# Kernel tuning notes

Hardware: AMD Instinct MI355X
Metric: run time of the kernel (lower is better)

## Reference

```python
import jax, jax.numpy as jnp
import numpy as np

ENC, DEC, B, S = 1024, 1024, 32, 2048


def setup_inputs() -> dict:
    key = jax.random.key(0)
    k1, k2, k3, k4, k5, k6 = jax.random.split(key, 6)
    scale_attn = 1.0 / np.sqrt(ENC + DEC)
    return {
        "decoder_hidden": jax.random.normal(k1, (B, DEC), dtype=jnp.float32),
        "encoder_outputs": jax.random.normal(k2, (B, S, ENC), dtype=jnp.float32),
        "mask": jax.random.randint(k3, (B, S), 0, 2, dtype=jnp.int32),
        "W_attn": jax.random.normal(k4, (ENC + DEC, DEC), dtype=jnp.float32) * scale_attn,
        "b_attn": jax.random.normal(k5, (DEC,), dtype=jnp.float32) * 0.02,
        "v_w": jax.random.normal(k6, (DEC,), dtype=jnp.float32) * (1.0 / np.sqrt(DEC)),
    }


def reference(decoder_hidden, encoder_outputs, mask, W_attn, b_attn, v_w):
    # Split cat((dec_exp, enc)) @ W into two GEMMs (same math, no repeat/concat).
    dec_dim = decoder_hidden.shape[-1]
    W_dec = W_attn[:dec_dim]      # [DEC, DEC]
    W_enc = W_attn[dec_dim:]      # [ENC, DEC]
    dec_proj = decoder_hidden @ W_dec                      # [B, DEC]
    enc_proj = jnp.einsum("bse,ed->bsd", encoder_outputs, W_enc)  # [B, S, DEC]
    energy = jnp.tanh(dec_proj[:, None, :] + enc_proj + b_attn)   # [B, S, DEC]
    scores = jnp.einsum("bsd,d->bs", energy, v_w)                 # [B, S]
    scores = jnp.where(mask == 0, -1e9, scores)
    attn_weights = jax.nn.softmax(scores, axis=1)                 # [B, S]
    context = jnp.einsum("bs,bse->be", attn_weights, encoder_outputs)  # [B, ENC]
    return (context, attn_weights)
```

## Files before the change

kernel.cpp:

```cpp
#include <hip/hip_runtime.h>
#include <hip/hip_bf16.h>
#include <cstdint>


#define ENCD 1024
#define DECD 1024
#define BATCH 32
#define SEQ 2048
#define MTOT (BATCH * SEQ)
#define KDIM 1024
#define NDIM 1024

typedef __attribute__((ext_vector_type(4))) float f32x4;
typedef __attribute__((ext_vector_type(8))) __bf16 bf16x8;
typedef __attribute__((ext_vector_type(8))) unsigned short u16x8;

__device__ __forceinline__ unsigned short f2bf(float f) {
  unsigned int u = __builtin_bit_cast(unsigned int, f);
  u += 0x7fffu + ((u >> 16) & 1u);
  return (unsigned short)(u >> 16);
}

__device__ __forceinline__ float bf2f(unsigned short h) {
  return __builtin_bit_cast(float, (unsigned int)h << 16);
}

__device__ __forceinline__ void async_lds16(const unsigned short* g, unsigned short* l) {
  __builtin_amdgcn_global_load_lds(
      (const __attribute__((address_space(1))) unsigned int*)g,
      (__attribute__((address_space(3))) unsigned int*)l, 16, 0, 0);
}

__global__ void conv_bf16_k(const float* __restrict__ src, unsigned short* __restrict__ dst) {
  const long i = ((long)blockIdx.x * 256 + threadIdx.x) * 8;
  const f32x4 f0 = *(const f32x4*)(src + i);
  const f32x4 f1 = *(const f32x4*)(src + i + 4);
  u16x8 v;
  v[0] = f2bf(f0[0]); v[1] = f2bf(f0[1]); v[2] = f2bf(f0[2]); v[3] = f2bf(f0[3]);
  v[4] = f2bf(f1[0]); v[5] = f2bf(f1[1]); v[6] = f2bf(f1[2]); v[7] = f2bf(f1[3]);
  *(u16x8*)(dst + i) = v;
}

__global__ void wt_k(const float* __restrict__ W, unsigned short* __restrict__ Wt) {
  __shared__ unsigned short t[64][65];
  const int k0 = blockIdx.x * 64, n0 = blockIdx.y * 64;
  const int tx = threadIdx.x & 63, ty = threadIdx.x >> 6;
#pragma unroll
  for (int i = 0; i < 16; ++i) {
    const int k = ty + i * 4;
    t[k][tx] = f2bf(W[(long)(DECD + k0 + k) * NDIM + n0 + tx]);
  }
  __syncthreads();
#pragma unroll
  for (int i = 0; i < 16; ++i) {
    const int n = ty + i * 4;
    Wt[(long)(n0 + n) * KDIM + k0 + tx] = t[tx][n];
  }
}

__global__ __launch_bounds__(256) void prep_k(
    const float* __restrict__ dec, const float* __restrict__ enc,
    const float* __restrict__ W, const float* __restrict__ bias,
    float* __restrict__ dp, unsigned short* __restrict__ Wt,
    unsigned short* __restrict__ Abf) {
  const int gb = blockIdx.x;
  const int tid = threadIdx.x;
  if (gb < 128) {
    const int b = gb >> 2;
    const int n = (gb & 3) * 256 + tid;
    const float* d = dec + b * DECD;
    const float* w = W + n;
    float acc = bias[n];
#pragma unroll 8
    for (int k = 0; k < 1024; ++k) acc = fmaf(d[k], w[(size_t)k * NDIM], acc);
    dp[b * NDIM + n] = acc;
  } else if (gb < 384) {
    __shared__ unsigned short t[64][65];
    const int g2 = gb - 128;
    const int k0 = (g2 & 15) * 64, n0 = (g2 >> 4) * 64;
    const int tx = tid & 63, ty = tid >> 6;
#pragma unroll
    for (int i = 0; i < 16; ++i) {
      const int k = ty + i * 4;
      t[k][tx] = f2bf(W[(size_t)(DECD + k0 + k) * NDIM + n0 + tx]);
    }
    __syncthreads();
#pragma unroll
    for (int i = 0; i < 16; ++i) {
      const int n = ty + i * 4;
      Wt[(size_t)(n0 + n) * KDIM + k0 + tx] = t[tx][n];
    }
  } else {
    const int cb = gb - 384;
#pragma unroll
    for (int k = 0; k < 16; ++k) {
      const long i = (((long)cb + (long)k * 2048) * 256 + tid) * 8;
      const f32x4 f0 = *(const f32x4*)(enc + i);
      const f32x4 f1 = *(const f32x4*)(enc + i + 4);
      u16x8 v;
      v[0] = f2bf(f0[0]); v[1] = f2bf(f0[1]); v[2] = f2bf(f0[2]); v[3] = f2bf(f0[3]);
      v[4] = f2bf(f1[0]); v[5] = f2bf(f1[1]); v[6] = f2bf(f1[2]); v[7] = f2bf(f1[3]);
      *(u16x8*)(Abf + i) = v;
    }
  }
}

__global__ __launch_bounds__(256, 4) void gemm_fast(
    const unsigned short* __restrict__ Abf, const unsigned short* __restrict__ Wt,
    const float* __restrict__ dp, const float* __restrict__ vw,
    float* __restrict__ sp) {
  __shared__ unsigned short sA[128 * 64];
  __shared__ unsigned short sB[128 * 64];

  const int tid = threadIdx.x;
  const int lane = tid & 63;
  const int wave = tid >> 6;
  const int wm = wave >> 1, wn = wave & 1;
  const int quad = lane >> 4;
  const int l15 = lane & 15;

  const int f = blockIdx.x + (blockIdx.y << 3);
  const int xcd = f & 7;
  const int c = f >> 3;
  const int bn = c & 7;
  const int bm = xcd + ((c >> 3) << 3);
  const int n0 = bn * 128;
  const int row0 = bm * 128;
  const int bidx = bm >> 4;

  const int srow = lane >> 3;
  const int schunk = (lane & 7) ^ srow;

  const f32x4 zz = {0.f, 0.f, 0.f, 0.f};
  f32x4 acc[4][4];
#pragma unroll
  for (int i = 0; i < 4; ++i)
#pragma unroll
    for (int j = 0; j < 4; ++j) acc[i][j] = zz;

  for (int kt = 0; kt < 16; ++kt) {
    const int k0 = kt * 64;
    __syncthreads();
#pragma unroll
    for (int i = 0; i < 4; ++i) {
      const int r = wave * 32 + i * 8 + srow;
      async_lds16(Abf + (size_t)(row0 + r) * KDIM + k0 + schunk * 8,
                  &sA[(wave * 32 + i * 8) * 64]);
      async_lds16(Wt + (size_t)(n0 + r) * KDIM + k0 + schunk * 8,
                  &sB[(wave * 32 + i * 8) * 64]);
    }
    __syncthreads();
#pragma unroll
    for (int h = 0; h < 2; ++h) {
      bf16x8 af[4], bf[4];
      const int slot = ((h * 4 + quad) ^ (l15 & 7)) * 8;
#pragma unroll
      for (int t = 0; t < 4; ++t) {
        af[t] = __builtin_bit_cast(bf16x8, *(const u16x8*)&sA[(wm * 64 + t * 16 + l15) * 64 + slot]);
        bf[t] = __builtin_bit_cast(bf16x8, *(const u16x8*)&sB[(wn * 64 + t * 16 + l15) * 64 + slot]);
      }
#pragma unroll
      for (int mt = 0; mt < 4; ++mt)
#pragma unroll
        for (int nt = 0; nt < 4; ++nt)
          acc[mt][nt] = __builtin_amdgcn_mfma_f32_16x16x32_bf16(
              af[mt], bf[nt], acc[mt][nt], 0, 0, 0);
    }
  }

  float vv[4], dv[4];
#pragma unroll
  for (int nt = 0; nt < 4; ++nt) {
    const int n = n0 + wn * 64 + nt * 16 + l15;
    vv[nt] = vw[n];
    dv[nt] = dp[bidx * NDIM + n];
  }
  float s_arr[4][4];
#pragma unroll
  for (int mt = 0; mt < 4; ++mt) {
#pragma unroll
    for (int r = 0; r < 4; ++r) {
      float s = 0.f;
#pragma unroll
      for (int nt = 0; nt < 4; ++nt) {
        float x = acc[mt][nt][r] + dv[nt];
        x = fminf(fmaxf(x, -10.f), 10.f);
        const float e = __expf(2.f * x);
        s += (e - 1.f) * __builtin_amdgcn_rcpf(e + 1.f) * vv[nt];
      }
      s += __shfl_xor(s, 1);
      s += __shfl_xor(s, 2);
      s += __shfl_xor(s, 4);
      s += __shfl_xor(s, 8);
      s_arr[mt][r] = s;
    }
  }
  __syncthreads();
  float* sRed = (float*)sA;
  if (wn == 1 && l15 == 0) {
#pragma unroll
    for (int mt = 0; mt < 4; ++mt)
#pragma unroll
      for (int r = 0; r < 4; ++r)
        sRed[wm * 64 + mt * 16 + quad * 4 + r] = s_arr[mt][r];
  }
  __syncthreads();
  if (wn == 0 && l15 == 0) {
#pragma unroll
    for (int mt = 0; mt < 4; ++mt)
#pragma unroll
      for (int r = 0; r < 4; ++r) {
        const int ml = wm * 64 + mt * 16 + quad * 4 + r;
        sp[(size_t)bn * MTOT + row0 + ml] = s_arr[mt][r] + sRed[ml];
      }
  }
}

__global__ __launch_bounds__(256) void sm_ctx_k(
    const float* __restrict__ sp, const int* __restrict__ mask,
    const unsigned short* __restrict__ Abf,
    float* __restrict__ attn, float* __restrict__ ctx) {
  __shared__ float a_s[SEQ];
  __shared__ float red[16][16][8];
  __shared__ float redm[4], reds[4];
  const int ec = blockIdx.x;
  const int b = blockIdx.y;
  const int tid = threadIdx.x;
  const int w = tid >> 6;
  const int* mrow = mask + b * SEQ;
  float vals[8];
  float mx = -3.0e38f;
#pragma unroll
  for (int i = 0; i < 8; ++i) {
    const int s = tid + i * 256;
    float v = 0.f;
#pragma unroll
    for (int p = 0; p < 8; ++p) v += sp[(size_t)p * MTOT + b * SEQ + s];
    if (mrow[s] == 0) v = -1.0e9f;
    vals[i] = v;
    mx = fmaxf(mx, v);
  }
#pragma unroll
  for (int off = 1; off < 64; off <<= 1) mx = fmaxf(mx, __shfl_xor(mx, off));
  if ((tid & 63) == 0) redm[w] = mx;
  __syncthreads();
  mx = fmaxf(fmaxf(redm[0], redm[1]), fmaxf(redm[2], redm[3]));
  float sum = 0.f;
#pragma unroll
  for (int i = 0; i < 8; ++i) {
    vals[i] = __expf(vals[i] - mx);
    sum += vals[i];
  }
#pragma unroll
  for (int off = 1; off < 64; off <<= 1) sum += __shfl_xor(sum, off);
  if ((tid & 63) == 0) reds[w] = sum;
  __syncthreads();
  sum = reds[0] + reds[1] + reds[2] + reds[3];
  const float inv = 1.0f / sum;
#pragma unroll
  for (int i = 0; i < 8; ++i) {
    const float av = vals[i] * inv;
    a_s[tid + i * 256] = av;
    if (ec == 0) attn[b * SEQ + tid + i * 256] = av;
  }
  __syncthreads();
  const int sg = tid >> 4, es = tid & 15;
  const int e0 = ec * 128 + es * 8;
  const unsigned short* base = Abf + (size_t)(b * SEQ) * ENCD + e0;
  float acc[8] = {0.f, 0.f, 0.f, 0.f, 0.f, 0.f, 0.f, 0.f};
#pragma unroll 4
  for (int k = 0; k < 128; ++k) {
    const int s = sg + k * 16;
    const float wgt = a_s[s];
    const u16x8 v = *(const u16x8*)(base + (size_t)s * ENCD);
#pragma unroll
    for (int j = 0; j < 8; ++j) acc[j] = fmaf(wgt, bf2f(v[j]), acc[j]);
  }
#pragma unroll
  for (int j = 0; j < 8; ++j) red[sg][es][j] = acc[j];
  __syncthreads();
  if (tid < 128) {
    const int es2 = tid >> 3, j = tid & 7;
    float ssum = 0.f;
#pragma unroll
    for (int g = 0; g < 16; ++g) ssum += red[g][es2][j];
    ctx[b * ENCD + ec * 128 + es2 * 8 + j] = ssum;
  }
}

__global__ void dec_proj_k2(const float* __restrict__ dec, const float* __restrict__ W,
                            float* __restrict__ dp) {
  const int idx = blockIdx.x * 256 + threadIdx.x;
  const int kc = blockIdx.y;
  const int b = idx >> 10;
  const int n = idx & 1023;
  const float* d = dec + b * DECD + kc * 128;
  const float* w = W + (long)(kc * 128) * NDIM + n;
  float acc = 0.f;
#pragma unroll 8
  for (int k = 0; k < 128; ++k) acc = fmaf(d[k], w[(long)k * NDIM], acc);
  atomicAdd(&dp[idx], acc);
}

__global__ __launch_bounds__(256, 3) void gemm_scores_bf16(
    const unsigned short* __restrict__ Abf, const unsigned short* __restrict__ Wt,
    const float* __restrict__ dp, const float* __restrict__ bias,
    const float* __restrict__ vw, float* __restrict__ scores) {
  __shared__ unsigned short sA[128 * 64];
  __shared__ unsigned short sB[128 * 64];
  const int tid = threadIdx.x;
  const int lane = tid & 63;
  const int wave = tid >> 6;
  const int wm = wave >> 1, wn = wave & 1;
  const int quad = lane >> 4;
  const int l15 = lane & 15;
  const int bn = blockIdx.x, bm = blockIdx.y;
  const int n0 = bn * 128, row0 = bm * 128, bidx = bm >> 4;
  const int srow = lane >> 3;
  const int schunk = (lane & 7) ^ srow;
  const f32x4 zz = {0.f, 0.f, 0.f, 0.f};
  f32x4 acc[4][4];
#pragma unroll
  for (int i = 0; i < 4; ++i)
#pragma unroll
    for (int j = 0; j < 4; ++j) acc[i][j] = zz;
  for (int kt = 0; kt < 16; ++kt) {
    const int k0 = kt * 64;
    __syncthreads();
#pragma unroll
    for (int i = 0; i < 4; ++i) {
      const int r = wave * 32 + i * 8 + srow;
      async_lds16(Abf + (size_t)(row0 + r) * KDIM + k0 + schunk * 8,
                  &sA[(wave * 32 + i * 8) * 64]);
      async_lds16(Wt + (size_t)(n0 + r) * KDIM + k0 + schunk * 8,
                  &sB[(wave * 32 + i * 8) * 64]);
    }
    __syncthreads();
#pragma unroll
    for (int h = 0; h < 2; ++h) {
      bf16x8 af[4], bf[4];
      const int slot = ((h * 4 + quad) ^ (l15 & 7)) * 8;
#pragma unroll
      for (int t = 0; t < 4; ++t) {
        af[t] = __builtin_bit_cast(bf16x8, *(const u16x8*)&sA[(wm * 64 + t * 16 + l15) * 64 + slot]);
        bf[t] = __builtin_bit_cast(bf16x8, *(const u16x8*)&sB[(wn * 64 + t * 16 + l15) * 64 + slot]);
      }
#pragma unroll
      for (int mt = 0; mt < 4; ++mt)
#pragma unroll
        for (int nt = 0; nt < 4; ++nt)
          acc[mt][nt] = __builtin_amdgcn_mfma_f32_16x16x32_bf16(
              af[mt], bf[nt], acc[mt][nt], 0, 0, 0);
    }
  }
  float vv[4], dv[4];
#pragma unroll
  for (int nt = 0; nt < 4; ++nt) {
    const int n = n0 + wn * 64 + nt * 16 + l15;
    vv[nt] = vw[n];
    dv[nt] = dp[bidx * NDIM + n] + bias[n];
  }
#pragma unroll
  for (int mt = 0; mt < 4; ++mt) {
#pragma unroll
    for (int r = 0; r < 4; ++r) {
      float s = 0.f;
#pragma unroll
      for (int nt = 0; nt < 4; ++nt) {
        float x = acc[mt][nt][r] + dv[nt];
        x = fminf(fmaxf(x, -10.f), 10.f);
        const float e = __expf(2.f * x);
        s += (e - 1.f) * __builtin_amdgcn_rcpf(e + 1.f) * vv[nt];
      }
      s += __shfl_xor(s, 1);
      s += __shfl_xor(s, 2);
      s += __shfl_xor(s, 4);
      s += __shfl_xor(s, 8);
      if (l15 == 0) atomicAdd(&scores[row0 + wm * 64 + mt * 16 + quad * 4 + r], s);
    }
  }
}

__global__ __launch_bounds__(256, 2) void gemm_scores_f32(
    const float* __restrict__ Ag, const unsigned short* __restrict__ Wt,
    const float* __restrict__ dp, const float* __restrict__ bias,
    const float* __restrict__ vw, float* __restrict__ scores) {
  __shared__ unsigned short sA[128 * 64];
  __shared__ unsigned short sB[128 * 64];
  const int tid = threadIdx.x;
  const int lane = tid & 63;
  const int wave = tid >> 6;
  const int wm = wave >> 1, wn = wave & 1;
  const int quad = lane >> 4;
  const int l15 = lane & 15;
  const int bn = blockIdx.x, bm = blockIdx.y;
  const int n0 = bn * 128, row0 = bm * 128, bidx = bm >> 4;
  const int sr = tid >> 3, sc = tid & 7;
  const f32x4 zz = {0.f, 0.f, 0.f, 0.f};
  f32x4 acc[4][4];
#pragma unroll
  for (int i = 0; i < 4; ++i)
#pragma unroll
    for (int j = 0; j < 4; ++j) acc[i][j] = zz;
  for (int kt = 0; kt < 16; ++kt) {
    const int k0 = kt * 64;
    __syncthreads();
#pragma unroll
    for (int j = 0; j < 4; ++j) {
      const int r = sr + 32 * j;
      const int c = sc ^ (r & 7);
      const float* src = Ag + (long)(row0 + r) * KDIM + (k0 + c * 8);
      f32x4 f0 = *(const f32x4*)src;
      f32x4 f1 = *(const f32x4*)(src + 4);
      u16x8 v;
      v[0] = f2bf(f0[0]); v[1] = f2bf(f0[1]); v[2] = f2bf(f0[2]); v[3] = f2bf(f0[3]);
      v[4] = f2bf(f1[0]); v[5] = f2bf(f1[1]); v[6] = f2bf(f1[2]); v[7] = f2bf(f1[3]);
      *(u16x8*)&sA[r * 64 + sc * 8] = v;
      *(u16x8*)&sB[r * 64 + sc * 8] = *(const u16x8*)(Wt + (long)(n0 + r) * KDIM + (k0 + c * 8));
    }
    __syncthreads();
#pragma unroll
    for (int h = 0; h < 2; ++h) {
      const int cs = ((h * 4 + quad) ^ (lane & 7)) * 8;
      bf16x8 af[4], bf[4];
#pragma unroll
      for (int t = 0; t < 4; ++t) {
        af[t] = __builtin_bit_cast(bf16x8, *(const u16x8*)&sA[(wm * 64 + t * 16 + l15) * 64 + cs]);
        bf[t] = __builtin_bit_cast(bf16x8, *(const u16x8*)&sB[(wn * 64 + t * 16 + l15) * 64 + cs]);
      }
#pragma unroll
      for (int mt = 0; mt < 4; ++mt)
#pragma unroll
        for (int nt = 0; nt < 4; ++nt)
          acc[mt][nt] = __builtin_amdgcn_mfma_f32_16x16x32_bf16(
              af[mt], bf[nt], acc[mt][nt], 0, 0, 0);
    }
  }
  float vv[4], dv[4];
#pragma unroll
  for (int nt = 0; nt < 4; ++nt) {
    const int n = n0 + wn * 64 + nt * 16 + l15;
    vv[nt] = vw[n];
    dv[nt] = dp[bidx * NDIM + n] + bias[n];
  }
#pragma unroll
  for (int mt = 0; mt < 4; ++mt) {
#pragma unroll
    for (int r = 0; r < 4; ++r) {
      float s = 0.f;
#pragma unroll
      for (int nt = 0; nt < 4; ++nt) {
        float x = acc[mt][nt][r] + dv[nt];
        x = fminf(fmaxf(x, -10.f), 10.f);
        const float e = __expf(2.f * x);
        s += (e - 1.f) * __builtin_amdgcn_rcpf(e + 1.f) * vv[nt];
      }
      s += __shfl_xor(s, 1);
      s += __shfl_xor(s, 2);
      s += __shfl_xor(s, 4);
      s += __shfl_xor(s, 8);
      if (l15 == 0) atomicAdd(&scores[row0 + wm * 64 + mt * 16 + quad * 4 + r], s);
    }
  }
}

__global__ void softmax_k(float* __restrict__ sc, const int* __restrict__ mask) {
  const int b = blockIdx.x;
  const int tid = threadIdx.x;
  const int w = tid >> 6;
  __shared__ float redm[4], reds[4];
  float* row = sc + b * SEQ;
  const int* mrow = mask + b * SEQ;
  float vals[8];
  float mx = -3.0e38f;
#pragma unroll
  for (int i = 0; i < 8; ++i) {
    const int s = tid + i * 256;
    float v = row[s];
    if (mrow[s] == 0) v = -1.0e9f;
    vals[i] = v;
    mx = fmaxf(mx, v);
  }
#pragma unroll
  for (int off = 1; off < 64; off <<= 1) mx = fmaxf(mx, __shfl_xor(mx, off));
  if ((tid & 63) == 0) redm[w] = mx;
  __syncthreads();
  mx = fmaxf(fmaxf(redm[0], redm[1]), fmaxf(redm[2], redm[3]));
  float sum = 0.f;
#pragma unroll
  for (int i = 0; i < 8; ++i) {
    vals[i] = __expf(vals[i] - mx);
    sum += vals[i];
  }
#pragma unroll
  for (int off = 1; off < 64; off <<= 1) sum += __shfl_xor(sum, off);
  if ((tid & 63) == 0) reds[w] = sum;
  __syncthreads();
  sum = reds[0] + reds[1] + reds[2] + reds[3];
  const float inv = 1.0f / sum;
#pragma unroll
  for (int i = 0; i < 8; ++i) row[tid + i * 256] = vals[i] * inv;
}

__global__ void context_k(const float* __restrict__ attn, const float* __restrict__ enc,
                          float* __restrict__ ctx) {
  const int b = blockIdx.y;
  const int s0 = blockIdx.x * 32;
  const int e = threadIdx.x * 4;
  const float* arow = attn + b * SEQ + s0;
  const float* ebase = enc + (long)(b * SEQ + s0) * ENCD + e;
  f32x4 acc = {0.f, 0.f, 0.f, 0.f};
#pragma unroll 8
  for (int s = 0; s < 32; ++s) {
    const float w = arow[s];
    const f32x4 v = *(const f32x4*)(ebase + (long)s * ENCD);
    acc += w * v;
  }
  float* dst = ctx + b * ENCD + e;
  atomicAdd(dst + 0, acc[0]);
  atomicAdd(dst + 1, acc[1]);
  atomicAdd(dst + 2, acc[2]);
  atomicAdd(dst + 3, acc[3]);
}

extern "C" void kernel_launch(void* const* d_in, const int* in_sizes, int n_in,
                              void* d_out, int out_size, void* d_ws, size_t ws_size,
                              hipStream_t stream) {
  (void)in_sizes; (void)n_in; (void)out_size;
  const float* dec  = (const float*)d_in[0];
  const float* enc  = (const float*)d_in[1];
  const int*   mask = (const int*)d_in[2];
  const float* W    = (const float*)d_in[3];
  const float* bias = (const float*)d_in[4];
  const float* vw   = (const float*)d_in[5];

  float* ctx  = (float*)d_out;
  float* attn = (float*)d_out + BATCH * ENCD;
  unsigned short* Wt  = (unsigned short*)d_ws;
  unsigned short* Abf = (unsigned short*)((char*)d_ws + (2ull << 20));
  float* shared = (float*)((char*)d_ws + (130ull << 20));

  const size_t needA = (132ull << 20);
  const size_t needB = (2ull << 20) + ((size_t)MTOT * KDIM * 2);

  if (ws_size >= needA) {
    prep_k<<<384 + 2048, 256, 0, stream>>>(dec, enc, W, bias, ctx, Wt, Abf);
    gemm_fast<<<dim3(8, 512), 256, 0, stream>>>(Abf, Wt, ctx, vw, shared);
    sm_ctx_k<<<dim3(8, 32), 256, 0, stream>>>(shared, mask, Abf, attn, ctx);
  } else if (ws_size >= needB) {
    wt_k<<<dim3(16, 16), 256, 0, stream>>>(W, Wt);
    hipMemsetAsync(attn, 0, (size_t)MTOT * sizeof(float), stream);
    hipMemsetAsync(ctx, 0, (size_t)(BATCH * NDIM) * sizeof(float), stream);
    dec_proj_k2<<<dim3(128, 8), 256, 0, stream>>>(dec, W, ctx);
    conv_bf16_k<<<32768, 256, 0, stream>>>(enc, Abf);
    gemm_scores_bf16<<<dim3(8, 512), 256, 0, stream>>>(Abf, Wt, ctx, bias, vw, attn);
    softmax_k<<<32, 256, 0, stream>>>(attn, mask);
    hipMemsetAsync(ctx, 0, (size_t)(BATCH * ENCD) * sizeof(float), stream);
    context_k<<<dim3(64, 32), 256, 0, stream>>>(attn, enc, ctx);
  } else {
    wt_k<<<dim3(16, 16), 256, 0, stream>>>(W, Wt);
    hipMemsetAsync(attn, 0, (size_t)MTOT * sizeof(float), stream);
    hipMemsetAsync(ctx, 0, (size_t)(BATCH * NDIM) * sizeof(float), stream);
    dec_proj_k2<<<dim3(128, 8), 256, 0, stream>>>(dec, W, ctx);
    gemm_scores_f32<<<dim3(8, 512), 256, 0, stream>>>(enc, Wt, ctx, bias, vw, attn);
    softmax_k<<<32, 256, 0, stream>>>(attn, mask);
    hipMemsetAsync(ctx, 0, (size_t)(BATCH * ENCD) * sizeof(float), stream);
    context_k<<<dim3(64, 32), 256, 0, stream>>>(attn, enc, ctx);
  }
}
```

Baseline: 595.1 us.

## Split softmax and context into separate kernels with sequence-split partial sums

Replaces the fused softmax+context kernel, which recomputed the softmax in each of 8 blocks per batch row, with a per-row softmax kernel, a context kernel that splits the sequence into 16 chunks writing partial sums, and a small reduction kernel. The enc-to-bf16 conversion in prep is also reshaped from 16 elements-chunks per thread over 2048 blocks to one chunk per thread over 32768 blocks. The goal is more parallelism in the context stage and no redundant softmax work. The cost is two extra kernel launches and a partial-sum round trip through memory.

```diff
diff --git a/kernel.cpp b/kernel.cpp
--- a/kernel.cpp
+++ b/kernel.cpp
@@ -91,17 +91,13 @@
       Wt[(size_t)(n0 + n) * KDIM + k0 + tx] = t[tx][n];
     }
   } else {
-    const int cb = gb - 384;
-#pragma unroll
-    for (int k = 0; k < 16; ++k) {
-      const long i = (((long)cb + (long)k * 2048) * 256 + tid) * 8;
-      const f32x4 f0 = *(const f32x4*)(enc + i);
-      const f32x4 f1 = *(const f32x4*)(enc + i + 4);
-      u16x8 v;
-      v[0] = f2bf(f0[0]); v[1] = f2bf(f0[1]); v[2] = f2bf(f0[2]); v[3] = f2bf(f0[3]);
-      v[4] = f2bf(f1[0]); v[5] = f2bf(f1[1]); v[6] = f2bf(f1[2]); v[7] = f2bf(f1[3]);
-      *(u16x8*)(Abf + i) = v;
-    }
+    const long i = ((long)(gb - 384) * 256 + tid) * 8;
+    const f32x4 f0 = *(const f32x4*)(enc + i);
+    const f32x4 f1 = *(const f32x4*)(enc + i + 4);
+    u16x8 v;
+    v[0] = f2bf(f0[0]); v[1] = f2bf(f0[1]); v[2] = f2bf(f0[2]); v[3] = f2bf(f0[3]);
+    v[4] = f2bf(f1[0]); v[5] = f2bf(f1[1]); v[6] = f2bf(f1[2]); v[7] = f2bf(f1[3]);
+    *(u16x8*)(Abf + i) = v;
   }
 }
 
@@ -216,17 +212,12 @@
   }
 }
 
-__global__ __launch_bounds__(256) void sm_ctx_k(
-    const float* __restrict__ sp, const int* __restrict__ mask,
-    const unsigned short* __restrict__ Abf,
-    float* __restrict__ attn, float* __restrict__ ctx) {
-  __shared__ float a_s[SEQ];
-  __shared__ float red[16][16][8];
-  __shared__ float redm[4], reds[4];
-  const int ec = blockIdx.x;
-  const int b = blockIdx.y;
+__global__ void softmax_part_k(const float* __restrict__ sp, const int* __restrict__ mask,
+                               float* __restrict__ attn) {
+  const int b = blockIdx.x;
   const int tid = threadIdx.x;
   const int w = tid >> 6;
+  __shared__ float redm[4], reds[4];
   const int* mrow = mask + b * SEQ;
   float vals[8];
   float mx = -3.0e38f;
@@ -235,7 +226,7 @@
     const int s = tid + i * 256;
     float v = 0.f;
 #pragma unroll
-    for (int p = 0; p < 8; ++p) v += sp[(size_t)p * MTOT + b * SEQ + s];
+    for (int bn = 0; bn < 8; ++bn) v += sp[(size_t)bn * MTOT + b * SEQ + s];
     if (mrow[s] == 0) v = -1.0e9f;
     vals[i] = v;
     mx = fmaxf(mx, v);
@@ -258,34 +249,35 @@
   sum = reds[0] + reds[1] + reds[2] + reds[3];
   const float inv = 1.0f / sum;
 #pragma unroll
-  for (int i = 0; i < 8; ++i) {
-    const float av = vals[i] * inv;
-    a_s[tid + i * 256] = av;
-    if (ec == 0) attn[b * SEQ + tid + i * 256] = av;
-  }
-  __syncthreads();
-  const int sg = tid >> 4, es = tid & 15;
-  const int e0 = ec * 128 + es * 8;
-  const unsigned short* base = Abf + (size_t)(b * SEQ) * ENCD + e0;
+  for (int i = 0; i < 8; ++i) attn[b * SEQ + tid + i * 256] = vals[i] * inv;
+}
+
+__global__ void ctx1_k(const float* __restrict__ attn, const unsigned short* __restrict__ Abf,
+                       float* __restrict__ part) {
+  const int sc = blockIdx.x;
+  const int b = blockIdx.y;
+  const int e0 = threadIdx.x * 8;
+  const float* arow = attn + b * SEQ + sc * 128;
+  const unsigned short* base = Abf + (size_t)(b * SEQ + sc * 128) * ENCD + e0;
   float acc[8] = {0.f, 0.f, 0.f, 0.f, 0.f, 0.f, 0.f, 0.f};
-#pragma unroll 4
-  for (int k = 0; k < 128; ++k) {
-    const int s = sg + k * 16;
-    const float wgt = a_s[s];
+#pragma unroll 8
+  for (int s = 0; s < 128; ++s) {
+    const float w = arow[s];
     const u16x8 v = *(const u16x8*)(base + (size_t)s * ENCD);
 #pragma unroll
-    for (int j = 0; j < 8; ++j) acc[j] = fmaf(wgt, bf2f(v[j]), acc[j]);
-  }
-#pragma unroll
-  for (int j = 0; j < 8; ++j) red[sg][es][j] = acc[j];
-  __syncthreads();
-  if (tid < 128) {
-    const int es2 = tid >> 3, j = tid & 7;
-    float ssum = 0.f;
-#pragma unroll
-    for (int g = 0; g < 16; ++g) ssum += red[g][es2][j];
-    ctx[b * ENCD + ec * 128 + es2 * 8 + j] = ssum;
-  }
+    for (int j = 0; j < 8; ++j) acc[j] = fmaf(w, bf2f(v[j]), acc[j]);
+  }
+  float* dst = part + (size_t)sc * (BATCH * ENCD) + b * ENCD + e0;
+  *(f32x4*)dst = *(f32x4*)&acc[0];
+  *(f32x4*)(dst + 4) = *(f32x4*)&acc[4];
+}
+
+__global__ void ctx2_k(const float* __restrict__ part, float* __restrict__ ctx) {
+  const int i = blockIdx.x * 256 + threadIdx.x;
+  float s = 0.f;
+#pragma unroll
+  for (int c = 0; c < 16; ++c) s += part[(size_t)c * (BATCH * ENCD) + i];
+  ctx[i] = s;
 }
 
 __global__ void dec_proj_k2(const float* __restrict__ dec, const float* __restrict__ W,
@@ -544,9 +536,11 @@
   const size_t needB = (2ull << 20) + ((size_t)MTOT * KDIM * 2);
 
   if (ws_size >= needA) {
-    prep_k<<<384 + 2048, 256, 0, stream>>>(dec, enc, W, bias, ctx, Wt, Abf);
+    prep_k<<<384 + 32768, 256, 0, stream>>>(dec, enc, W, bias, ctx, Wt, Abf);
     gemm_fast<<<dim3(8, 512), 256, 0, stream>>>(Abf, Wt, ctx, vw, shared);
-    sm_ctx_k<<<dim3(8, 32), 256, 0, stream>>>(shared, mask, Abf, attn, ctx);
+    softmax_part_k<<<32, 256, 0, stream>>>(shared, mask, attn);
+    ctx1_k<<<dim3(16, 32), 128, 0, stream>>>(attn, Abf, shared);
+    ctx2_k<<<128, 256, 0, stream>>>(shared, ctx);
   } else if (ws_size >= needB) {
     wt_k<<<dim3(16, 16), 256, 0, stream>>>(W, Wt);
     hipMemsetAsync(attn, 0, (size_t)MTOT * sizeof(float), stream);
```

Measured after the change: 584.3 us. About the same (-1.8%).
